# Kernel tuning notes

Measured on AMD Instinct MI355X. Metric: run time of the kernel, lower is better.

## Reference

```python
import jax, jax.numpy as jnp
import numpy as np

N_NODES = 50000
N_EDGES = 800000
IN_CH, HID, HEADS, OUT_CH = 16, 64, 4, 8
NEG_SLOPE = 0.2


def _add_self_loops(edge_index, num_nodes):
    loop = jnp.arange(num_nodes, dtype=edge_index.dtype)
    loops = jnp.stack([loop, loop])  # [2, N]
    return jnp.concatenate([edge_index, loops], axis=1)


def _gat_conv(x, src, dst, W, a_src, a_dst, bias, concat):
    """PyG-style GATConv: linear -> per-edge LeakyReLU attention -> segment
    softmax over incoming edges -> scatter-add aggregate."""
    N = x.shape[0]
    H, C = a_src.shape
    h = (x @ W).reshape(N, H, C)                      # [N,H,C]
    alpha_src = (h * a_src).sum(-1)                   # [N,H]
    alpha_dst = (h * a_dst).sum(-1)                   # [N,H]
    e = jax.nn.leaky_relu(alpha_src[src] + alpha_dst[dst], NEG_SLOPE)  # [E,H]
    # numerically stable segment softmax over edges grouped by dst
    e_max = jax.ops.segment_max(e, dst, num_segments=N)
    e_exp = jnp.exp(e - e_max[dst])
    denom = jax.ops.segment_sum(e_exp, dst, num_segments=N)
    alpha = e_exp / denom[dst]                        # [E,H]
    msg = h[src] * alpha[:, :, None]                  # [E,H,C]
    out = jax.ops.segment_sum(msg, dst, num_segments=N)  # [N,H,C]
    if concat:
        return out.reshape(N, H * C) + bias
    return out.mean(axis=1) + bias


def setup_inputs() -> dict:
    key = jax.random.key(0)
    ks = jax.random.split(key, 12)
    s = 0.1
    return {
        "x": jax.random.normal(ks[0], (N_NODES, IN_CH), jnp.float32),
        "edge_index": jax.random.randint(ks[1], (2, N_EDGES), 0, N_NODES, jnp.int64),
        "W1": jax.random.normal(ks[2], (IN_CH, HEADS * HID), jnp.float32) * s,
        "as1": jax.random.normal(ks[3], (HEADS, HID), jnp.float32) * s,
        "ad1": jax.random.normal(ks[4], (HEADS, HID), jnp.float32) * s,
        "b1": jnp.zeros((HEADS * HID,), jnp.float32),
        "W2": jax.random.normal(ks[5], (HEADS * HID, HEADS * HID), jnp.float32) * s,
        "as2": jax.random.normal(ks[6], (HEADS, HID), jnp.float32) * s,
        "ad2": jax.random.normal(ks[7], (HEADS, HID), jnp.float32) * s,
        "b2": jnp.zeros((HID,), jnp.float32),
        "Wc": jax.random.normal(ks[8], (HID, OUT_CH), jnp.float32) * s,
        "bc": jnp.zeros((OUT_CH,), jnp.float32),
    }


def reference(x, edge_index, W1, as1, ad1, b1, W2, as2, ad2, b2, Wc, bc):
    ei = _add_self_loops(edge_index, x.shape[0])
    src, dst = ei[0], ei[1]
    h = _gat_conv(x, src, dst, W1, as1, ad1, b1, concat=True)
    h = jax.nn.elu(h)
    h = _gat_conv(h, src, dst, W2, as2, ad2, b2, concat=False)
    h = jax.nn.elu(h)
    return h @ Wc + bc  # [N, OUT_CH]
```

## Files before the change

kernel.cpp:

```cpp
#include <hip/hip_runtime.h>
#include <math.h>

#define NODES   50000
#define HEADS   4
#define HID     64
#define FDIM    256
#define IN_CH   16
#define NEG_SLOPE 0.2f

typedef unsigned short ushort_t;
typedef unsigned int uint_t;
typedef __attribute__((ext_vector_type(8))) short bf16x8;
typedef __attribute__((ext_vector_type(4))) float f32x4;

__device__ inline ushort_t f2bf(float f) {
    uint_t u = __float_as_uint(f);
    u += 0x7fffu + ((u >> 16) & 1u);
    return (ushort_t)(u >> 16);
}
__device__ inline uint_t f2h(float f) {
    _Float16 h = (_Float16)f;
    return (uint_t)*(ushort_t*)&h;
}
__device__ inline float h2f(uint_t u) {
    ushort_t us = (ushort_t)u;
    _Float16 h = *(_Float16*)&us;
    return (float)h;
}

__device__ inline void fmamix8(float* a, uint4 hv, float pw) {
    asm("v_fma_mix_f32 %0, %8, %9, %0 op_sel:[0,0,0] op_sel_hi:[0,1,0]\n\t"
        "v_fma_mix_f32 %1, %8, %9, %1 op_sel:[0,1,0] op_sel_hi:[0,1,0]\n\t"
        "v_fma_mix_f32 %2, %8, %10, %2 op_sel:[0,0,0] op_sel_hi:[0,1,0]\n\t"
        "v_fma_mix_f32 %3, %8, %10, %3 op_sel:[0,1,0] op_sel_hi:[0,1,0]\n\t"
        "v_fma_mix_f32 %4, %8, %11, %4 op_sel:[0,0,0] op_sel_hi:[0,1,0]\n\t"
        "v_fma_mix_f32 %5, %8, %11, %5 op_sel:[0,1,0] op_sel_hi:[0,1,0]\n\t"
        "v_fma_mix_f32 %6, %8, %12, %6 op_sel:[0,0,0] op_sel_hi:[0,1,0]\n\t"
        "v_fma_mix_f32 %7, %8, %12, %7 op_sel:[0,1,0] op_sel_hi:[0,1,0]"
        : "+v"(a[0]), "+v"(a[1]), "+v"(a[2]), "+v"(a[3]),
          "+v"(a[4]), "+v"(a[5]), "+v"(a[6]), "+v"(a[7])
        : "v"(pw), "v"(hv.x), "v"(hv.y), "v"(hv.z), "v"(hv.w));
}


__global__ __launch_bounds__(256) void k_prep(const float* __restrict__ x,
                                              const float* __restrict__ W1,
                                              const float* __restrict__ as1,
                                              const float* __restrict__ ad1,
                                              const float* __restrict__ W2,
                                              const int* __restrict__ ei, int E,
                                              ushort_t* __restrict__ h,
                                              float* __restrict__ asrc,
                                              float* __restrict__ adst,
                                              ushort_t* __restrict__ W2T,
                                              int* __restrict__ deg, int Nn, int NB) {
    int bid = blockIdx.x, t = threadIdx.x;
    if (bid >= NB + 256) {
        int e = (bid - NB - 256) * 256 + t;
        int Etot = E + Nn;
        if (e >= Etot) return;
        int d = (e < E) ? ei[E + e] : (e - E);
        if (d >= 0 && d < Nn) atomicAdd(&deg[d], 1);
        return;
    }
    if (bid >= NB) {
        int idx = (bid - NB) * 256 + t;
        int n = idx >> 8, k = idx & 255;
        W2T[idx] = f2bf(W2[k * FDIM + n]);
        return;
    }
    float w1c[16];
#pragma unroll
    for (int k = 0; k < 16; ++k) w1c[k] = W1[k * FDIM + t];
    float av = as1[t], dv = ad1[t];
    int hh = t >> 6;
#pragma unroll
    for (int j = 0; j < 8; ++j) {
        int n = bid * 8 + j;
        if (n >= Nn) break;
        const float4* xp = (const float4*)(x + n * IN_CH);
        float4 x0 = xp[0], x1 = xp[1], x2 = xp[2], x3 = xp[3];
        float s = x0.x * w1c[0]  + x0.y * w1c[1]  + x0.z * w1c[2]  + x0.w * w1c[3]
                + x1.x * w1c[4]  + x1.y * w1c[5]  + x1.z * w1c[6]  + x1.w * w1c[7]
                + x2.x * w1c[8]  + x2.y * w1c[9]  + x2.z * w1c[10] + x2.w * w1c[11]
                + x3.x * w1c[12] + x3.y * w1c[13] + x3.z * w1c[14] + x3.w * w1c[15];
        uint_t pv = f2h(s);
        uint_t ov = __shfl_down(pv, 1);
        if (!(t & 1)) *(uint_t*)(h + (long)n * FDIM + t) = pv | (ov << 16);
        float p1 = s * av, p2 = s * dv;
#pragma unroll
        for (int off = 1; off < 64; off <<= 1) {
            p1 += __shfl_xor(p1, off);
            p2 += __shfl_xor(p2, off);
        }
        if ((t & 63) == 0) {
            asrc[n * 4 + hh] = p1;
            adst[n * 4 + hh] = p2;
        }
    }
}


__global__ __launch_bounds__(256) void k_scanA(const int* __restrict__ deg,
                                               int* __restrict__ bsum, int N) {
    __shared__ int sh[256];
    int t = threadIdx.x;
    int i0 = blockIdx.x * 4096 + t * 16;
    int s = 0;
#pragma unroll
    for (int j = 0; j < 16; ++j) s += (i0 + j < N) ? deg[i0 + j] : 0;
    sh[t] = s;
    __syncthreads();
    for (int off = 128; off; off >>= 1) {
        if (t < off) sh[t] += sh[t + off];
        __syncthreads();
    }
    if (t == 0) bsum[blockIdx.x] = sh[0];
}

__global__ void k_scanB(int* __restrict__ bsum, int* __restrict__ rowst, int nb, int N) {
    int t = threadIdx.x;
    int orig = (t < nb) ? bsum[t] : 0;
    int v = orig;
#pragma unroll
    for (int off = 1; off < 64; off <<= 1) {
        int u = __shfl_up(v, off);
        if (t >= off) v += u;
    }
    if (t < nb) bsum[t] = v - orig;
    if (t == 63) rowst[N] = v;
}

__global__ __launch_bounds__(256) void k_scanC(const int* __restrict__ deg,
                                               const int* __restrict__ bsum,
                                               int* __restrict__ rowst,
                                               int* __restrict__ cursor, int N) {
    __shared__ int sh[256];
    int t = threadIdx.x, b = blockIdx.x;
    int i0 = b * 4096 + t * 16;
    int v[16], s = 0;
#pragma unroll
    for (int j = 0; j < 16; ++j) { v[j] = (i0 + j < N) ? deg[i0 + j] : 0; s += v[j]; }
    sh[t] = s;
    __syncthreads();
    for (int off = 1; off < 256; off <<= 1) {
        int u = (t >= off) ? sh[t - off] : 0;
        __syncthreads();
        sh[t] += u;
        __syncthreads();
    }
    int excl = sh[t] - s + bsum[b];
#pragma unroll
    for (int j = 0; j < 16; ++j) {
        if (i0 + j < N) { rowst[i0 + j] = excl; cursor[i0 + j] = excl; }
        excl += v[j];
    }
}

__global__ void k_scatter(const int* __restrict__ ei, int E, int N,
                          int* __restrict__ cursor, int2* __restrict__ csr2) {
    int e = blockIdx.x * blockDim.x + threadIdx.x;
    int Etot = E + N;
    if (e >= Etot) return;
    int s, d;
    if (e < E) { s = ei[e]; d = ei[E + e]; } else { s = d = e - E; }
    if (d < 0 || d >= N) return;
    int pos = atomicAdd(&cursor[d], 1);
    csr2[pos] = make_int2(s, d);
}


__global__ __launch_bounds__(256) void k_gemm2(const ushort_t* __restrict__ A,
                                               const ushort_t* __restrict__ BT,
                                               const float* __restrict__ as2,
                                               const float* __restrict__ ad2,
                                               ushort_t* __restrict__ C,
                                               float* __restrict__ asrc,
                                               float* __restrict__ adst, int M) {
    __shared__ short As[64 * 40];
    __shared__ short Bs[64 * 40];
    __shared__ float2 red[64][2];
    int tid = threadIdx.x;
    int row0 = blockIdx.y * 64, col0 = blockIdx.x * 64;
    int wid = tid >> 6, lane = tid & 63;
    int wm = wid >> 1, wn = wid & 1;
    int quad = lane >> 4, lm = lane & 15;
    int lr = tid >> 2, lk = (tid & 3) * 8;
    f32x4 acc[2][2] = {};
    for (int k0 = 0; k0 < FDIM; k0 += 32) {
        uint4 av = {0u, 0u, 0u, 0u};
        int ar = row0 + lr;
        if (ar < M) av = *(const uint4*)(A + (long)ar * FDIM + k0 + lk);
        *(uint4*)(&As[lr * 40 + lk]) = av;
        uint4 bv = *(const uint4*)(BT + (long)(col0 + lr) * FDIM + k0 + lk);
        *(uint4*)(&Bs[lr * 40 + lk]) = bv;
        __syncthreads();
        bf16x8 a0 = *(const bf16x8*)(&As[(wm * 32 + lm) * 40 + quad * 8]);
        bf16x8 a1 = *(const bf16x8*)(&As[(wm * 32 + 16 + lm) * 40 + quad * 8]);
        bf16x8 b0 = *(const bf16x8*)(&Bs[(wn * 32 + lm) * 40 + quad * 8]);
        bf16x8 b1 = *(const bf16x8*)(&Bs[(wn * 32 + 16 + lm) * 40 + quad * 8]);
        acc[0][0] = __builtin_amdgcn_mfma_f32_16x16x32_bf16(a0, b0, acc[0][0], 0, 0, 0);
        acc[0][1] = __builtin_amdgcn_mfma_f32_16x16x32_bf16(a0, b1, acc[0][1], 0, 0, 0);
        acc[1][0] = __builtin_amdgcn_mfma_f32_16x16x32_bf16(a1, b0, acc[1][0], 0, 0, 0);
        acc[1][1] = __builtin_amdgcn_mfma_f32_16x16x32_bf16(a1, b1, acc[1][1], 0, 0, 0);
        __syncthreads();
    }
#pragma unroll
    for (int mi = 0; mi < 2; ++mi)
#pragma unroll
        for (int ni = 0; ni < 2; ++ni)
#pragma unroll
            for (int r = 0; r < 4; ++r) {
                int row = row0 + wm * 32 + mi * 16 + quad * 4 + r;
                int col = col0 + wn * 32 + ni * 16 + lm;
                if (row < M) C[(long)row * FDIM + col] = (ushort_t)f2h(acc[mi][ni][r]);
            }
    float asv0 = as2[col0 + wn * 32 + lm], asv1 = as2[col0 + wn * 32 + 16 + lm];
    float adv0 = ad2[col0 + wn * 32 + lm], adv1 = ad2[col0 + wn * 32 + 16 + lm];
#pragma unroll
    for (int mi = 0; mi < 2; ++mi)
#pragma unroll
        for (int r = 0; r < 4; ++r) {
            float ps = acc[mi][0][r] * asv0 + acc[mi][1][r] * asv1;
            float pd = acc[mi][0][r] * adv0 + acc[mi][1][r] * adv1;
#pragma unroll
            for (int off = 1; off < 16; off <<= 1) {
                ps += __shfl_xor(ps, off);
                pd += __shfl_xor(pd, off);
            }
            if (lm == 0) red[wm * 32 + mi * 16 + quad * 4 + r][wn] = make_float2(ps, pd);
        }
    __syncthreads();
    if (tid < 64) {
        int row = row0 + tid;
        if (row < M) {
            float2 e0 = red[tid][0], e1 = red[tid][1];
            asrc[row * 4 + blockIdx.x] = e0.x + e1.x;
            adst[row * 4 + blockIdx.x] = e0.y + e1.y;
        }
    }
}


__global__ void k_pw(const int2* __restrict__ csr2, const float* __restrict__ asrc,
                     const float* __restrict__ adst, uint_t* __restrict__ pwb, int Etot) {
    int e = blockIdx.x * blockDim.x + threadIdx.x;
    if (e >= Etot) return;
    int2 sd = csr2[e];
    float4 av = *(const float4*)(asrc + sd.x * 4);
    float4 dv = *(const float4*)(adst + sd.y * 4);
    float t[4] = {av.x + dv.x, av.y + dv.y, av.z + dv.z, av.w + dv.w};
    uint_t sh = (uint_t)sd.x << 16;
#pragma unroll
    for (int h = 0; h < 4; ++h) {
        float tt = (t[h] > 0.f) ? t[h] : NEG_SLOPE * t[h];
        pwb[h * Etot + e] = sh | f2h(__expf(tt));
    }
}


__global__ __launch_bounds__(256) void k_agg(const ushort_t* __restrict__ h,
                                             const uint_t* __restrict__ pwb,
                                             const int* __restrict__ row_start,
                                             const float* __restrict__ b1,
                                             const float* __restrict__ b2,
                                             const float* __restrict__ Wc,
                                             const float* __restrict__ bc,
                                             ushort_t* __restrict__ hout,
                                             float* __restrict__ fout,
                                             int mode, int Etot, int N) {
    __shared__ float zsh[2 * FDIM];
    __shared__ float wsh[584];
    int tid  = threadIdx.x;
    int hh   = tid >> 6;
    int lane = tid & 63;
    int half = lane >> 5;
    int l32  = lane & 31;
    int g    = l32 >> 3;
    int cg   = l32 & 7;
    int d    = blockIdx.x * 2 + half;
    bool valid = d < N;

    if (!mode) {
        for (int i = tid; i < 584; i += 256)
            wsh[i] = (i < 512) ? Wc[i] : ((i < 520) ? bc[i - 512] : b2[i - 520]);
    }

    int s0 = 0, s1 = 0;
    if (valid) { s0 = row_start[d]; s1 = row_start[d + 1]; }
    int cnt  = s1 - s0;
    int maxc = max(cnt, __shfl_xor(cnt, 32));

    const char* hb  = (const char*)h;
    const char* pwc = (const char*)pwb;
    uint_t loff  = ((uint_t)hh * HID + (uint_t)cg * 8) * 2;
    uint_t pbyte = ((uint_t)hh * (uint_t)Etot + (uint_t)(s0 + g)) << 2;

    float acc[8] = {0.f, 0.f, 0.f, 0.f, 0.f, 0.f, 0.f, 0.f};
    float den = 0.f;

    for (int off = 0; off < maxc; off += 16) {
        int i0 = s0 + off + g;
        uint_t pb = pbyte + ((uint_t)off << 2);
        uint_t u0 = (i0      < s1) ? *(const uint_t*)(pwc + pb)      : 0u;
        uint_t u1 = (i0 + 4  < s1) ? *(const uint_t*)(pwc + pb + 16) : 0u;
        uint_t u2 = (i0 + 8  < s1) ? *(const uint_t*)(pwc + pb + 32) : 0u;
        uint_t u3 = (i0 + 12 < s1) ? *(const uint_t*)(pwc + pb + 48) : 0u;
        uint4 hv0 = *(const uint4*)(hb + (((u0 >> 16) << 9) + loff));
        uint4 hv1 = *(const uint4*)(hb + (((u1 >> 16) << 9) + loff));
        uint4 hv2 = *(const uint4*)(hb + (((u2 >> 16) << 9) + loff));
        uint4 hv3 = *(const uint4*)(hb + (((u3 >> 16) << 9) + loff));
        float pw0 = h2f(u0), pw1 = h2f(u1);
        float pw2 = h2f(u2), pw3 = h2f(u3);
        den += (pw0 + pw1) + (pw2 + pw3);
        fmamix8(acc, hv0, pw0);
        fmamix8(acc, hv1, pw1);
        fmamix8(acc, hv2, pw2);
        fmamix8(acc, hv3, pw3);
    }
#pragma unroll
    for (int off = 8; off <= 16; off <<= 1) {
#pragma unroll
        for (int j = 0; j < 8; ++j) acc[j] += __shfl_xor(acc[j], off);
        den += __shfl_xor(den, off);
    }

    if (mode) {
        if (g == 0 && valid) {
            float inv = 1.f / den;
            const float* bp = b1 + hh * HID + cg * 8;
            float v[8];
#pragma unroll
            for (int j = 0; j < 8; ++j) {
                float t = acc[j] * inv + bp[j];
                v[j] = (t > 0.f) ? t : __expf(t) - 1.f;
            }
            uint4 u;
            u.x = (uint_t)f2bf(v[0]) | ((uint_t)f2bf(v[1]) << 16);
            u.y = (uint_t)f2bf(v[2]) | ((uint_t)f2bf(v[3]) << 16);
            u.z = (uint_t)f2bf(v[4]) | ((uint_t)f2bf(v[5]) << 16);
            u.w = (uint_t)f2bf(v[6]) | ((uint_t)f2bf(v[7]) << 16);
            *(uint4*)(hout + (long)d * FDIM + hh * HID + cg * 8) = u;
        }
    } else {
        if (g == 0 && valid) {
            float inv = 1.f / den;
            int zb = half * FDIM + hh * HID + cg * 8;
#pragma unroll
            for (int j = 0; j < 8; ++j) zsh[zb + j] = acc[j] * inv;
        }
        __syncthreads();
        if (tid < 128) {
            int node = tid >> 6, c = tid & 63;
            int dd = blockIdx.x * 2 + node;
            if (dd < N) {
                const float* zp = zsh + node * FDIM;
                float zv = 0.25f * (zp[c] + zp[64 + c] + zp[128 + c] + zp[192 + c])
                         + wsh[520 + c];
                zv = (zv > 0.f) ? zv : __expf(zv) - 1.f;
                zsh[node * FDIM + c] = zv;
            }
        }
        __syncthreads();
        if (tid < 16) {
            int node = tid >> 3, o = tid & 7;
            int dd = blockIdx.x * 2 + node;
            if (dd < N) {
                float acc2 = wsh[512 + o];
                const float* zp = zsh + node * FDIM;
#pragma unroll 8
                for (int c = 0; c < 64; ++c) acc2 += zp[c] * wsh[c * 8 + o];
                fout[(long)dd * 8 + o] = acc2;
            }
        }
    }
}


extern "C" void kernel_launch(void* const* d_in, const int* in_sizes, int n_in,
                              void* d_out, int out_size, void* d_ws, size_t ws_size,
                              hipStream_t stream) {
    const float* x   = (const float*)d_in[0];
    const int*   ei  = (const int*)d_in[1];
    const float* W1  = (const float*)d_in[2];
    const float* as1 = (const float*)d_in[3];
    const float* ad1 = (const float*)d_in[4];
    const float* b1  = (const float*)d_in[5];
    const float* W2  = (const float*)d_in[6];
    const float* as2 = (const float*)d_in[7];
    const float* ad2 = (const float*)d_in[8];
    const float* b2  = (const float*)d_in[9];
    const float* Wc  = (const float*)d_in[10];
    const float* bc  = (const float*)d_in[11];
    float* out = (float*)d_out;

    const int N = NODES;
    const int E = in_sizes[1] / 2;
    const int Etot = E + N;

    char* ws = (char*)d_ws;
    size_t off = 0;
    auto alloc = [&](size_t bytes) {
        void* p = ws + off;
        off = (off + bytes + 255) & ~(size_t)255;
        return p;
    };
    ushort_t* hbf    = (ushort_t*)alloc((size_t)N * FDIM * 2);
    ushort_t* hact   = (ushort_t*)alloc((size_t)N * FDIM * 2);
    float*    asrc   = (float*)alloc((size_t)N * HEADS * 4);
    float*    adst   = (float*)alloc((size_t)N * HEADS * 4);
    ushort_t* W2T    = (ushort_t*)alloc((size_t)FDIM * FDIM * 2);
    int*      deg    = (int*)alloc((size_t)N * 4);
    int*      rowst  = (int*)alloc((size_t)(N + 1) * 4);
    int*      cursor = (int*)alloc((size_t)N * 4);
    int*      bsum   = (int*)alloc(64 * 4);
    int2*     csr2   = (int2*)alloc((size_t)Etot * 8);
    uint_t*   pwb    = (uint_t*)alloc((size_t)Etot * HEADS * 4);

    const int tpb = 256;
    int egrid = (Etot + tpb - 1) / tpb;
    int nb = (N + 4095) / 4096;
    int NB = (N + 7) / 8;

    hipMemsetAsync(deg, 0, (size_t)N * 4, stream);

    k_prep<<<NB + 256 + egrid, tpb, 0, stream>>>(x, W1, as1, ad1, W2, ei, E,
                                                 hbf, asrc, adst, W2T, deg, N, NB);
    k_scanA<<<nb, 256, 0, stream>>>(deg, bsum, N);
    k_scanB<<<1, 64, 0, stream>>>(bsum, rowst, nb, N);
    k_scanC<<<nb, 256, 0, stream>>>(deg, bsum, rowst, cursor, N);
    k_scatter<<<egrid, tpb, 0, stream>>>(ei, E, N, cursor, csr2);

    k_pw<<<egrid, tpb, 0, stream>>>(csr2, asrc, adst, pwb, Etot);
    k_agg<<<(N + 1) / 2, 256, 0, stream>>>(hbf, pwb, rowst, b1, nullptr, nullptr, nullptr,
                                           hact, nullptr, 1, Etot, N);

    dim3 g2(FDIM / 64, (N + 63) / 64);
    k_gemm2<<<g2, 256, 0, stream>>>(hact, W2T, as2, ad2, hbf, asrc, adst, N);
    k_pw<<<egrid, tpb, 0, stream>>>(csr2, asrc, adst, pwb, Etot);
    k_agg<<<(N + 1) / 2, 256, 0, stream>>>(hbf, pwb, rowst, nullptr, b2, Wc, bc,
                                           nullptr, out, 0, Etot, N);
}
```

Before: 383.5 us.

## Store node features head-major and split aggregation per head for gather locality

The projected features are now stored in a head-major layout ([head][node][64]) by both the first-layer projection and the second GEMM. Each aggregation block now handles one head for eight nodes, so the gathered rows come from a 6.4 MB per-head slice instead of the full 25.6 MB table, which should improve L2 hit rates on random gathers. Edge-weight loads and output stores become nontemporal. The second-layer head-mean, ELU and classifier move into a separate k_fin kernel that reads an fp16 intermediate, which costs one extra launch and a round trip through memory.

```diff
diff --git a/kernel.cpp b/kernel.cpp
--- a/kernel.cpp
+++ b/kernel.cpp
@@ -12,6 +12,7 @@
 typedef unsigned int uint_t;
 typedef __attribute__((ext_vector_type(8))) short bf16x8;
 typedef __attribute__((ext_vector_type(4))) float f32x4;
+typedef __attribute__((ext_vector_type(4))) uint_t u32x4;
 
 __device__ inline ushort_t f2bf(float f) {
     uint_t u = __float_as_uint(f);
@@ -86,7 +87,8 @@
                 + x3.x * w1c[12] + x3.y * w1c[13] + x3.z * w1c[14] + x3.w * w1c[15];
         uint_t pv = f2h(s);
         uint_t ov = __shfl_down(pv, 1);
-        if (!(t & 1)) *(uint_t*)(h + (long)n * FDIM + t) = pv | (ov << 16);
+        if (!(t & 1))
+            *(uint_t*)(h + (((long)hh * Nn + n) << 6) + (t & 63)) = pv | (ov << 16);
         float p1 = s * av, p2 = s * dv;
 #pragma unroll
         for (int off = 1; off < 64; off <<= 1) {
@@ -212,8 +214,9 @@
 #pragma unroll
             for (int r = 0; r < 4; ++r) {
                 int row = row0 + wm * 32 + mi * 16 + quad * 4 + r;
-                int col = col0 + wn * 32 + ni * 16 + lm;
-                if (row < M) C[(long)row * FDIM + col] = (ushort_t)f2h(acc[mi][ni][r]);
+                int colw = wn * 32 + ni * 16 + lm;
+                if (row < M)
+                    C[(((long)blockIdx.x * M + row) << 6) + colw] = (ushort_t)f2h(acc[mi][ni][r]);
             }
     float asv0 = as2[col0 + wn * 32 + lm], asv1 = as2[col0 + wn * 32 + 16 + lm];
     float adv0 = ad2[col0 + wn * 32 + lm], adv1 = ad2[col0 + wn * 32 + 16 + lm];
@@ -263,38 +266,31 @@
                                              const uint_t* __restrict__ pwb,
                                              const int* __restrict__ row_start,
                                              const float* __restrict__ b1,
-                                             const float* __restrict__ b2,
-                                             const float* __restrict__ Wc,
-                                             const float* __restrict__ bc,
                                              ushort_t* __restrict__ hout,
-                                             float* __restrict__ fout,
+                                             ushort_t* __restrict__ zn,
                                              int mode, int Etot, int N) {
-    __shared__ float zsh[2 * FDIM];
-    __shared__ float wsh[584];
     int tid  = threadIdx.x;
-    int hh   = tid >> 6;
+    int bid  = blockIdx.x;
+    int head = bid & 3;
+    int nb   = bid >> 2;
+    int wv   = tid >> 6;
     int lane = tid & 63;
     int half = lane >> 5;
     int l32  = lane & 31;
     int g    = l32 >> 3;
     int cg   = l32 & 7;
-    int d    = blockIdx.x * 2 + half;
+    int d    = nb * 8 + wv * 2 + half;
     bool valid = d < N;
-
-    if (!mode) {
-        for (int i = tid; i < 584; i += 256)
-            wsh[i] = (i < 512) ? Wc[i] : ((i < 520) ? bc[i - 512] : b2[i - 520]);
-    }
 
     int s0 = 0, s1 = 0;
     if (valid) { s0 = row_start[d]; s1 = row_start[d + 1]; }
     int cnt  = s1 - s0;
     int maxc = max(cnt, __shfl_xor(cnt, 32));
 
-    const char* hb  = (const char*)h;
+    const char* hb  = (const char*)h + ((size_t)head * (size_t)N << 7);
     const char* pwc = (const char*)pwb;
-    uint_t loff  = ((uint_t)hh * HID + (uint_t)cg * 8) * 2;
-    uint_t pbyte = ((uint_t)hh * (uint_t)Etot + (uint_t)(s0 + g)) << 2;
+    uint_t loff  = (uint_t)cg * 16;
+    uint_t pbyte = ((uint_t)head * (uint_t)Etot + (uint_t)(s0 + g)) << 2;
 
     float acc[8] = {0.f, 0.f, 0.f, 0.f, 0.f, 0.f, 0.f, 0.f};
     float den = 0.f;
@@ -302,14 +298,14 @@
     for (int off = 0; off < maxc; off += 16) {
         int i0 = s0 + off + g;
         uint_t pb = pbyte + ((uint_t)off << 2);
-        uint_t u0 = (i0      < s1) ? *(const uint_t*)(pwc + pb)      : 0u;
-        uint_t u1 = (i0 + 4  < s1) ? *(const uint_t*)(pwc + pb + 16) : 0u;
-        uint_t u2 = (i0 + 8  < s1) ? *(const uint_t*)(pwc + pb + 32) : 0u;
-        uint_t u3 = (i0 + 12 < s1) ? *(const uint_t*)(pwc + pb + 48) : 0u;
-        uint4 hv0 = *(const uint4*)(hb + (((u0 >> 16) << 9) + loff));
-        uint4 hv1 = *(const uint4*)(hb + (((u1 >> 16) << 9) + loff));
-        uint4 hv2 = *(const uint4*)(hb + (((u2 >> 16) << 9) + loff));
-        uint4 hv3 = *(const uint4*)(hb + (((u3 >> 16) << 9) + loff));
+        uint_t u0 = (i0      < s1) ? __builtin_nontemporal_load((const uint_t*)(pwc + pb))      : 0u;
+        uint_t u1 = (i0 + 4  < s1) ? __builtin_nontemporal_load((const uint_t*)(pwc + pb + 16)) : 0u;
+        uint_t u2 = (i0 + 8  < s1) ? __builtin_nontemporal_load((const uint_t*)(pwc + pb + 32)) : 0u;
+        uint_t u3 = (i0 + 12 < s1) ? __builtin_nontemporal_load((const uint_t*)(pwc + pb + 48)) : 0u;
+        uint4 hv0 = *(const uint4*)(hb + (((u0 >> 16) << 7) + loff));
+        uint4 hv1 = *(const uint4*)(hb + (((u1 >> 16) << 7) + loff));
+        uint4 hv2 = *(const uint4*)(hb + (((u2 >> 16) << 7) + loff));
+        uint4 hv3 = *(const uint4*)(hb + (((u3 >> 16) << 7) + loff));
         float pw0 = h2f(u0), pw1 = h2f(u1);
         float pw2 = h2f(u2), pw3 = h2f(u3);
         den += (pw0 + pw1) + (pw2 + pw3);
@@ -325,53 +321,64 @@
         den += __shfl_xor(den, off);
     }
 
+    if (g != 0 || !valid) return;
+    float inv = 1.f / den;
     if (mode) {
-        if (g == 0 && valid) {
-            float inv = 1.f / den;
-            const float* bp = b1 + hh * HID + cg * 8;
-            float v[8];
-#pragma unroll
-            for (int j = 0; j < 8; ++j) {
-                float t = acc[j] * inv + bp[j];
-                v[j] = (t > 0.f) ? t : __expf(t) - 1.f;
-            }
-            uint4 u;
-            u.x = (uint_t)f2bf(v[0]) | ((uint_t)f2bf(v[1]) << 16);
-            u.y = (uint_t)f2bf(v[2]) | ((uint_t)f2bf(v[3]) << 16);
-            u.z = (uint_t)f2bf(v[4]) | ((uint_t)f2bf(v[5]) << 16);
-            u.w = (uint_t)f2bf(v[6]) | ((uint_t)f2bf(v[7]) << 16);
-            *(uint4*)(hout + (long)d * FDIM + hh * HID + cg * 8) = u;
-        }
+        const float* bp = b1 + head * HID + cg * 8;
+        float v[8];
+#pragma unroll
+        for (int j = 0; j < 8; ++j) {
+            float t = acc[j] * inv + bp[j];
+            v[j] = (t > 0.f) ? t : __expf(t) - 1.f;
+        }
+        u32x4 u;
+        u.x = (uint_t)f2bf(v[0]) | ((uint_t)f2bf(v[1]) << 16);
+        u.y = (uint_t)f2bf(v[2]) | ((uint_t)f2bf(v[3]) << 16);
+        u.z = (uint_t)f2bf(v[4]) | ((uint_t)f2bf(v[5]) << 16);
+        u.w = (uint_t)f2bf(v[6]) | ((uint_t)f2bf(v[7]) << 16);
+        __builtin_nontemporal_store(u, (u32x4*)(hout + (long)d * FDIM + head * HID + cg * 8));
     } else {
-        if (g == 0 && valid) {
-            float inv = 1.f / den;
-            int zb = half * FDIM + hh * HID + cg * 8;
-#pragma unroll
-            for (int j = 0; j < 8; ++j) zsh[zb + j] = acc[j] * inv;
-        }
-        __syncthreads();
-        if (tid < 128) {
-            int node = tid >> 6, c = tid & 63;
-            int dd = blockIdx.x * 2 + node;
-            if (dd < N) {
-                const float* zp = zsh + node * FDIM;
-                float zv = 0.25f * (zp[c] + zp[64 + c] + zp[128 + c] + zp[192 + c])
-                         + wsh[520 + c];
-                zv = (zv > 0.f) ? zv : __expf(zv) - 1.f;
-                zsh[node * FDIM + c] = zv;
-            }
-        }
-        __syncthreads();
-        if (tid < 16) {
-            int node = tid >> 3, o = tid & 7;
-            int dd = blockIdx.x * 2 + node;
-            if (dd < N) {
-                float acc2 = wsh[512 + o];
-                const float* zp = zsh + node * FDIM;
+        u32x4 u;
+        u.x = f2h(acc[0] * inv) | (f2h(acc[1] * inv) << 16);
+        u.y = f2h(acc[2] * inv) | (f2h(acc[3] * inv) << 16);
+        u.z = f2h(acc[4] * inv) | (f2h(acc[5] * inv) << 16);
+        u.w = f2h(acc[6] * inv) | (f2h(acc[7] * inv) << 16);
+        __builtin_nontemporal_store(u, (u32x4*)(zn + (((long)head * N + d) << 6) + cg * 8));
+    }
+}
+
+
+__global__ __launch_bounds__(256) void k_fin(const ushort_t* __restrict__ zn,
+                                             const float* __restrict__ b2,
+                                             const float* __restrict__ Wc,
+                                             const float* __restrict__ bc,
+                                             float* __restrict__ out, int N) {
+    __shared__ float zsh[256];
+    __shared__ float wsh[584];
+    int tid = threadIdx.x;
+    for (int i = tid; i < 584; i += 256)
+        wsh[i] = (i < 512) ? Wc[i] : ((i < 520) ? bc[i - 512] : b2[i - 520]);
+    __syncthreads();
+    int ln = tid >> 6, c = tid & 63;
+    int n = blockIdx.x * 4 + ln;
+    if (n < N) {
+        long base = ((long)n << 6) + c;
+        long hs = (long)N << 6;
+        float v = 0.25f * (h2f(zn[base]) + h2f(zn[base + hs])
+                         + h2f(zn[base + 2 * hs]) + h2f(zn[base + 3 * hs]))
+                + wsh[520 + c];
+        zsh[ln * 64 + c] = (v > 0.f) ? v : __expf(v) - 1.f;
+    }
+    __syncthreads();
+    if (tid < 32) {
+        int ln2 = tid >> 3, o = tid & 7;
+        int nn = blockIdx.x * 4 + ln2;
+        if (nn < N) {
+            float acc = wsh[512 + o];
+            const float* zp = zsh + ln2 * 64;
 #pragma unroll 8
-                for (int c = 0; c < 64; ++c) acc2 += zp[c] * wsh[c * 8 + o];
-                fout[(long)dd * 8 + o] = acc2;
-            }
+            for (int c2 = 0; c2 < 64; ++c2) acc += zp[c2] * wsh[c2 * 8 + o];
+            out[(long)nn * 8 + o] = acc;
         }
     }
 }
@@ -416,11 +423,13 @@
     int*      bsum   = (int*)alloc(64 * 4);
     int2*     csr2   = (int2*)alloc((size_t)Etot * 8);
     uint_t*   pwb    = (uint_t*)alloc((size_t)Etot * HEADS * 4);
+    ushort_t* znorm  = hact;
 
     const int tpb = 256;
     int egrid = (Etot + tpb - 1) / tpb;
     int nb = (N + 4095) / 4096;
     int NB = (N + 7) / 8;
+    int agrid = 4 * ((N + 7) / 8);
 
     hipMemsetAsync(deg, 0, (size_t)N * 4, stream);
 
@@ -432,12 +441,11 @@
     k_scatter<<<egrid, tpb, 0, stream>>>(ei, E, N, cursor, csr2);
 
     k_pw<<<egrid, tpb, 0, stream>>>(csr2, asrc, adst, pwb, Etot);
-    k_agg<<<(N + 1) / 2, 256, 0, stream>>>(hbf, pwb, rowst, b1, nullptr, nullptr, nullptr,
-                                           hact, nullptr, 1, Etot, N);
+    k_agg<<<agrid, 256, 0, stream>>>(hbf, pwb, rowst, b1, hact, nullptr, 1, Etot, N);
 
     dim3 g2(FDIM / 64, (N + 63) / 64);
     k_gemm2<<<g2, 256, 0, stream>>>(hact, W2T, as2, ad2, hbf, asrc, adst, N);
     k_pw<<<egrid, tpb, 0, stream>>>(csr2, asrc, adst, pwb, Etot);
-    k_agg<<<(N + 1) / 2, 256, 0, stream>>>(hbf, pwb, rowst, nullptr, b2, Wc, bc,
-                                           nullptr, out, 0, Etot, N);
-}
+    k_agg<<<agrid, 256, 0, stream>>>(hbf, pwb, rowst, nullptr, nullptr, znorm, 0, Etot, N);
+    k_fin<<<(N + 3) / 4, 256, 0, stream>>>(znorm, b2, Wc, bc, out, N);
+}
```

After: 374.1 us. -2.5%, faster.
